# Kernel tuning notes

Measured on AMD Instinct MI355X. Metric: run time of the kernel, lower is better.

Reference implementation:

```python
import jax, jax.numpy as jnp
import numpy as np

L, B, T, TC, T1, D, DK, FF = 4, 4, 1024, 1024, 2048, 384, 256, 1536
TT = 0.1   # lamed blending coefficient (tt in (0,1] path)
EPS = 1e-5


def _ln(x, g, b):
    m = jnp.mean(x, axis=-1, keepdims=True)
    v = jnp.mean((x - m) ** 2, axis=-1, keepdims=True)
    return (x - m) * jax.lax.rsqrt(v + EPS) * g + b


def setup_inputs() -> dict:
    key = jax.random.key(0)
    ks = jax.random.split(key, 16)
    s = 0.02
    return {
        "tgt": jax.random.normal(ks[0], (B, T, D), jnp.float32),
        "memory": jax.random.normal(ks[1], (B, T1, DK), jnp.float32),
        "score_c": jax.random.normal(ks[2], (L, B, TC, T1), jnp.float32),
        "out_c": jax.random.normal(ks[3], (L, B, TC, D), jnp.float32),
        "Wq": jax.random.normal(ks[4], (L, D, D), jnp.float32) * s,
        "bq": jnp.zeros((L, D), jnp.float32),
        "Wk": jax.random.normal(ks[5], (L, D, DK), jnp.float32) * s,
        "bk": jnp.zeros((L, D), jnp.float32),
        "Wv": jax.random.normal(ks[6], (L, D, DK), jnp.float32) * s,
        "bv": jnp.zeros((L, D), jnp.float32),
        "Wkn": jax.random.normal(ks[7], (L, D, D), jnp.float32) * s,
        "bkn": jnp.zeros((L, D), jnp.float32),
        "Wun": jax.random.normal(ks[8], (L, D, D), jnp.float32) * s,
        "bun": jnp.zeros((L, D), jnp.float32),
        "W1": jax.random.normal(ks[9], (L, FF, D), jnp.float32) * s,
        "b1": jnp.zeros((L, FF), jnp.float32),
        "W2": jax.random.normal(ks[10], (L, D, FF), jnp.float32) * s,
        "b2": jnp.zeros((L, D), jnp.float32),
        "g1": jnp.ones((L, D), jnp.float32),
        "be1": jnp.zeros((L, D), jnp.float32),
        "g2": jnp.ones((L, D), jnp.float32),
        "be2": jnp.zeros((L, D), jnp.float32),
    }


def reference(tgt, memory, score_c, out_c, Wq, bq, Wk, bk, Wv, bv,
              Wkn, bkn, Wun, bun, W1, b1, W2, b2, g1, be1, g2, be2):
    scale = 1.0 / np.sqrt(D)
    x = tgt
    for l in range(L):  # fixed small layer count
        # cross-attention q/k/v (n_head = 1)
        q = jnp.einsum('btd,ed->bte', x, Wq[l]) + bq[l]            # [B,T,D]
        k = jnp.einsum('bsk,ek->bse', memory, Wk[l]) + bk[l]       # [B,T1,D]
        v = jnp.einsum('bsk,ek->bse', memory, Wv[l]) + bv[l]       # [B,T1,D]
        att = jnp.einsum('bte,bse->bts', q, k) * scale             # [B,T,T1]
        # blended score path (tt in (0,1])
        unk = jnp.einsum('btd,ed->bte', x, Wun[l]) + bun[l]        # [B,T,D]
        kno = jnp.einsum('bcd,ed->bce', out_c[l], Wkn[l]) + bkn[l] # [B,TC,D]
        score1 = jnp.einsum('bte,bce->btc', unk, kno) * scale      # [B,T,TC]
        mixed = jnp.einsum('btc,bcs->bts', score1, score_c[l])     # [B,T,T1]
        blended = TT * jax.nn.softmax(mixed, axis=-1) \
                  + (1.0 - TT) * jax.nn.softmax(att, axis=-1)
        z = jnp.einsum('bts,bse->bte', blended, v)                 # [B,T,D]
        x = _ln(x + z, g1[l], be1[l])
        h = jax.nn.relu(jnp.einsum('btd,fd->btf', x, W1[l]) + b1[l])
        y2 = jnp.einsum('btf,df->btd', h, W2[l]) + b2[l]
        x = _ln(x + y2, g2[l], be2[l])
    return x
```

## Files before the change

kernel.cpp:

```cpp
#include <hip/hip_runtime.h>
#include <math.h>

#define Lc 4
#define Bc 4
#define Tc 1024
#define TCc 1024
#define T1c 2048
#define Dc 384
#define DKc 256
#define FFc 1536
#define TTc 0.1f
#define EPSc 1e-5f

typedef unsigned short u16;
typedef __attribute__((ext_vector_type(8))) __bf16 bf16x8;
typedef __attribute__((ext_vector_type(8))) _Float16 f16x8;
typedef __attribute__((ext_vector_type(4))) float f32x4;

__device__ inline u16 f2bf(float f) {
  union { float f; unsigned u; } x; x.f = f;
  unsigned r = x.u + 0x7fffu + ((x.u >> 16) & 1u);
  return (u16)(r >> 16);
}

struct CDesc { const float* src; u16* dst; long n4; };
struct CPack { CDesc d[16]; long tot4; int nd; };

__global__ void cvt_multi(CPack P) {
  long i = (long)blockIdx.x * 256 + threadIdx.x;
  const long st = (long)gridDim.x * 256;
  for (; i < P.tot4; i += st) {
    long r = i; int g = 0;
    while (g < P.nd - 1 && r >= P.d[g].n4) { r -= P.d[g].n4; ++g; }
    float4 v = ((const float4*)P.d[g].src)[r];
    ushort4 o;
    o.x = f2bf(v.x); o.y = f2bf(v.y); o.z = f2bf(v.z); o.w = f2bf(v.w);
    ((ushort4*)P.d[g].dst)[r] = o;
  }
}

__global__ void concat_bias(const float* __restrict__ a, const float* __restrict__ b,
                            float* __restrict__ o) {
  int l = blockIdx.x, t = threadIdx.x;
  o[l * 768 + t] = (t < Dc) ? a[l * Dc + t] : b[l * Dc + t - Dc];
}

__global__ __launch_bounds__(256) void transpose_cvt(const float* __restrict__ src,
                                                     u16* __restrict__ dst) {
  __shared__ float t[64 * 65];
  const int z = blockIdx.z;
  const float* s = src + (long)z * TCc * T1c;
  u16* d = dst + (long)z * T1c * TCc;
  const int s0 = blockIdx.x * 64, c0 = blockIdx.y * 64;
  const int tc = threadIdx.x >> 4;
  const int tx = (threadIdx.x & 15) * 4;
#pragma unroll
  for (int it = 0; it < 4; ++it) {
    const int c = tc + it * 16;
    float4 v = *(const float4*)(s + (long)(c0 + c) * T1c + s0 + tx);
    float* q = t + c * 65 + tx;
    q[0] = v.x; q[1] = v.y; q[2] = v.z; q[3] = v.w;
  }
  __syncthreads();
#pragma unroll
  for (int it = 0; it < 4; ++it) {
    const int srow = tc + it * 16;
    u16 o[4];
#pragma unroll
    for (int k2 = 0; k2 < 4; ++k2) o[k2] = f2bf(t[(tx + k2) * 65 + srow]);
    *(ushort4*)(d + (long)(s0 + srow) * TCc + c0 + tx) = *(ushort4*)o;
  }
}

template<int BIAS_MODE, int RELU, int OUT_MODE, int SWIZ, int DUAL>
__global__ __launch_bounds__(256) void gemm_bt(
    const u16* __restrict__ A, const u16* __restrict__ B,
    void* __restrict__ C, const float* __restrict__ bias,
    float alpha, int N, int K, int lda, int ldb,
    long sA, long sB, long sC, long sBias, int ksplit, long sSlab, int bdivA,
    const u16* __restrict__ B2, int ldb2, long sB2, int aoff2,
    void* __restrict__ C2, float alpha2, int nbat)
{
  __shared__ __attribute__((aligned(16))) u16 As[2][128 * 32];
  __shared__ __attribute__((aligned(16))) u16 Bs[2][128 * 32];
  const int bz = blockIdx.z;
  int b = bz / ksplit;
  const int kc = bz - b * ksplit;
  const u16* Bp = B; int ldbv = ldb; long sBv = sB; void* Cp = C;
  int aoff = 0; float al = alpha;
  if (DUAL && b >= nbat) {
    b -= nbat; Bp = B2; ldbv = ldb2; sBv = sB2; Cp = C2; aoff = aoff2; al = alpha2;
  }
  const int ba = b / bdivA;
  const int Klen = K / ksplit;
  const int k0 = kc * Klen;
  const u16* Ab = A + (long)ba * sA + aoff;
  const u16* Bb = Bp + (long)b * sBv;
  long tm, tn;
  if (SWIZ) {
    const int id = blockIdx.y * 16 + blockIdx.x;
    tm = (long)(id >> 4) * 128;
    tn = (long)(2 * (id & 7) + ((id >> 3) & 1)) * 128;
  } else {
    tm = (long)blockIdx.y * 128; tn = (long)blockIdx.x * 128;
  }
  const int tid = threadIdx.x;
  const int lane = tid & 63, wv = tid >> 6;
  const int wm = (wv >> 1) * 64, wn = (wv & 1) * 64;
  const int q = lane >> 4, r = lane & 15;
  const int ldr = lane >> 2;
  const int ldc = (lane & 3) * 8;

  const u16* gA0 = Ab + (tm + wv * 32 + ldr) * (long)lda + k0 + ldc;
  const u16* gA1 = gA0 + 16 * (long)lda;
  const u16* gB0 = Bb + (tn + wv * 32 + ldr) * (long)ldbv + k0 + ldc;
  const u16* gB1 = gB0 + 16 * (long)ldbv;
  const int dof = (wv * 32 + ldr) * 32 + ldc;

  const f32x4 zero4 = {0.0f, 0.0f, 0.0f, 0.0f};
  f32x4 acc[4][4];
#pragma unroll
  for (int i = 0; i < 4; ++i)
#pragma unroll
    for (int j = 0; j < 4; ++j) acc[i][j] = zero4;

  uint4 ra0 = *(const uint4*)gA0;
  uint4 ra1 = *(const uint4*)gA1;
  uint4 rb0 = *(const uint4*)gB0;
  uint4 rb1 = *(const uint4*)gB1;

  const int iters = Klen >> 5;
  int cur = 0;
  for (int it = 0; it < iters; ++it) {
    u16* a0 = As[cur] + dof;
    u16* b0 = Bs[cur] + dof;
    *(uint4*)a0 = ra0; *(uint4*)(a0 + 512) = ra1;
    *(uint4*)b0 = rb0; *(uint4*)(b0 + 512) = rb1;
    if (it + 1 < iters) {
      const long o = (long)(it + 1) * 32;
      ra0 = *(const uint4*)(gA0 + o);
      ra1 = *(const uint4*)(gA1 + o);
      rb0 = *(const uint4*)(gB0 + o);
      rb1 = *(const uint4*)(gB1 + o);
    }
    __syncthreads();
    bf16x8 af[4], bfr[4];
#pragma unroll
    for (int i = 0; i < 4; ++i) {
      af[i]  = *(const bf16x8*)(As[cur] + (wm + i * 16 + r) * 32 + q * 8);
      bfr[i] = *(const bf16x8*)(Bs[cur] + (wn + i * 16 + r) * 32 + q * 8);
    }
#pragma unroll
    for (int i = 0; i < 4; ++i)
#pragma unroll
      for (int j = 0; j < 4; ++j)
        acc[i][j] = __builtin_amdgcn_mfma_f32_16x16x32_bf16(af[i], bfr[j], acc[i][j], 0, 0, 0);
    cur ^= 1;
  }

  const float* biasb = bias ? bias + (long)ba * sBias : nullptr;
#pragma unroll
  for (int i = 0; i < 4; ++i)
#pragma unroll
    for (int j = 0; j < 4; ++j)
#pragma unroll
      for (int v = 0; v < 4; ++v) {
        long row = tm + wm + i * 16 + q * 4 + v;
        long col = tn + wn + j * 16 + r;
        float val = acc[i][j][v] * al;
        if (BIAS_MODE == 1 && kc == 0) val += biasb[col];
        if (BIAS_MODE == 2 && kc == 0) val += biasb[row];
        if (RELU) val = fmaxf(val, 0.0f);
        long idx = (long)kc * sSlab + (long)b * sC + row * (long)N + col;
        if (OUT_MODE == 0)      ((float*)Cp)[idx] = val;
        else if (OUT_MODE == 1) ((u16*)Cp)[idx] = f2bf(val);
        else                    ((_Float16*)Cp)[idx] = (_Float16)val;
      }
}

__global__ __launch_bounds__(256) void blend_softmax(
    const _Float16* __restrict__ att, const _Float16* __restrict__ mixed,
    u16* __restrict__ out)
{
  const long row = blockIdx.x;
  const int tid = threadIdx.x;
  f16x8 av = *(const f16x8*)(att + row * T1c + tid * 8);
  f16x8 mv = *(const f16x8*)(mixed + row * T1c + tid * 8);
  float a[8], m[8];
#pragma unroll
  for (int i = 0; i < 8; ++i) { a[i] = (float)av[i]; m[i] = (float)mv[i]; }
  float amax = a[0], mmax = m[0];
#pragma unroll
  for (int i = 1; i < 8; ++i) { amax = fmaxf(amax, a[i]); mmax = fmaxf(mmax, m[i]); }
#pragma unroll
  for (int off = 32; off > 0; off >>= 1) {
    amax = fmaxf(amax, __shfl_xor(amax, off));
    mmax = fmaxf(mmax, __shfl_xor(mmax, off));
  }
  __shared__ float red[8];
  const int lane = tid & 63, wv = tid >> 6;
  if (lane == 0) { red[wv] = amax; red[4 + wv] = mmax; }
  __syncthreads();
  amax = fmaxf(fmaxf(red[0], red[1]), fmaxf(red[2], red[3]));
  mmax = fmaxf(fmaxf(red[4], red[5]), fmaxf(red[6], red[7]));
  __syncthreads();
  float asum = 0.f, msum = 0.f;
#pragma unroll
  for (int i = 0; i < 8; ++i) {
    a[i] = __expf(a[i] - amax); asum += a[i];
    m[i] = __expf(m[i] - mmax); msum += m[i];
  }
#pragma unroll
  for (int off = 32; off > 0; off >>= 1) {
    asum += __shfl_xor(asum, off);
    msum += __shfl_xor(msum, off);
  }
  if (lane == 0) { red[wv] = asum; red[4 + wv] = msum; }
  __syncthreads();
  asum = red[0] + red[1] + red[2] + red[3];
  msum = red[4] + red[5] + red[6] + red[7];
  const float ca = (1.0f - TTc) / asum, cm = TTc / msum;
  u16 o[8];
#pragma unroll
  for (int i = 0; i < 8; ++i) o[i] = f2bf(a[i] * ca + m[i] * cm);
  *(uint4*)(out + row * T1c + tid * 8) = *(uint4*)o;
}

__global__ __launch_bounds__(384) void add_ln4(
    const float* __restrict__ xin, const float* __restrict__ zs,
    const float* __restrict__ g, const float* __restrict__ be,
    float* __restrict__ xout, u16* __restrict__ xbf)
{
  const long row = blockIdx.x;
  const int d = threadIdx.x;
  const long SL = (long)Bc * Tc * Dc;
  const long o = row * Dc + d;
  float v = xin[o] + zs[o] + zs[SL + o] + zs[2 * SL + o] + zs[3 * SL + o];
  float s = v, s2 = v * v;
#pragma unroll
  for (int off = 32; off > 0; off >>= 1) {
    s  += __shfl_xor(s, off);
    s2 += __shfl_xor(s2, off);
  }
  __shared__ float red[12];
  const int lane = d & 63, wv = d >> 6;
  if (lane == 0) { red[wv] = s; red[6 + wv] = s2; }
  __syncthreads();
  float S = 0.f, S2 = 0.f;
#pragma unroll
  for (int w = 0; w < 6; ++w) { S += red[w]; S2 += red[6 + w]; }
  const float mean = S * (1.0f / Dc);
  const float var  = S2 * (1.0f / Dc) - mean * mean;
  const float rstd = rsqrtf(var + EPSc);
  const float y = (v - mean) * rstd * g[d] + be[d];
  xout[o] = y;
  xbf[o] = f2bf(y);
}

extern "C" void kernel_launch(void* const* d_in, const int* in_sizes, int n_in,
                              void* d_out, int out_size, void* d_ws, size_t ws_size,
                              hipStream_t stream)
{
  const float* tgt     = (const float*)d_in[0];
  const float* memory  = (const float*)d_in[1];
  const float* score_c = (const float*)d_in[2];
  const float* out_c   = (const float*)d_in[3];
  const float* Wq  = (const float*)d_in[4];  const float* bq  = (const float*)d_in[5];
  const float* Wk  = (const float*)d_in[6];  const float* bk  = (const float*)d_in[7];
  const float* Wv  = (const float*)d_in[8];  const float* bv  = (const float*)d_in[9];
  const float* Wkn = (const float*)d_in[10]; const float* bkn = (const float*)d_in[11];
  const float* Wun = (const float*)d_in[12]; const float* bun = (const float*)d_in[13];
  const float* W1  = (const float*)d_in[14]; const float* b1  = (const float*)d_in[15];
  const float* W2  = (const float*)d_in[16]; const float* b2  = (const float*)d_in[17];
  const float* g1  = (const float*)d_in[18]; const float* be1 = (const float*)d_in[19];
  const float* g2  = (const float*)d_in[20]; const float* be2 = (const float*)d_in[21];
  (void)in_sizes; (void)n_in; (void)out_size;

  char* p = (char*)d_ws;
  auto alloc = [&](size_t b) { char* r = p; p += (b + 255) & ~(size_t)255; return r; };

  u16* wk_bf   = (u16*)alloc((size_t)Lc * Dc * DKc * 2);
  u16* wv_bf   = (u16*)alloc((size_t)Lc * Dc * DKc * 2);
  u16* wkn_bf  = (u16*)alloc((size_t)Lc * Dc * Dc * 2);
  u16* w1_bf   = (u16*)alloc((size_t)Lc * FFc * Dc * 2);
  u16* w2_bf   = (u16*)alloc((size_t)Lc * Dc * FFc * 2);
  u16* wqu_bf  = (u16*)alloc((size_t)Lc * 2 * Dc * Dc * 2);
  float* bqu   = (float*)alloc((size_t)Lc * 2 * Dc * 4);
  u16* mem_bf  = (u16*)alloc((size_t)Bc * T1c * DKc * 2);
  u16* outc_bf = (u16*)alloc((size_t)Lc * Bc * TCc * Dc * 2);
  u16* x_bf    = (u16*)alloc((size_t)Bc * Tc * Dc * 2);
  float* xbuf  = (float*)alloc((size_t)Bc * Tc * Dc * 4);
  u16* qunk_bf = (u16*)alloc((size_t)Bc * Tc * 2 * Dc * 2);
  u16* k_all   = (u16*)alloc((size_t)Bc * T1c * Lc * Dc * 2);
  u16* vT_all  = (u16*)alloc((size_t)Bc * Lc * Dc * T1c * 2);
  u16* knoT_all = (u16*)alloc((size_t)Lc * Bc * Dc * TCc * 2);
  u16* M2T_all = (u16*)alloc((size_t)Lc * Bc * T1c * Dc * 2);
  u16* scT_all = (u16*)alloc((size_t)Lc * Bc * T1c * TCc * 2);
  _Float16* att   = (_Float16*)alloc((size_t)Bc * Tc * T1c * 2);
  _Float16* mixed = (_Float16*)alloc((size_t)Bc * Tc * T1c * 2);
  u16* blended = (u16*)alloc((size_t)Bc * Tc * T1c * 2);
  float* zslab = (float*)alloc((size_t)4 * Bc * Tc * Dc * 4);
  float* yslab = (float*)alloc((size_t)4 * Bc * Tc * Dc * 4);
  u16* h_bf    = (u16*)alloc((size_t)Bc * Tc * FFc * 2);

  if ((size_t)(p - (char*)d_ws) > ws_size) return;

  {
    CPack cp{}; int g = 0; long tot4 = 0;
    auto add = [&](const float* s, u16* d, long n) {
      cp.d[g].src = s; cp.d[g].dst = d; cp.d[g].n4 = n / 4; tot4 += n / 4; ++g;
    };
    add(Wk,  wk_bf,  (long)Lc * Dc * DKc);
    add(Wv,  wv_bf,  (long)Lc * Dc * DKc);
    add(Wkn, wkn_bf, (long)Lc * Dc * Dc);
    add(W1,  w1_bf,  (long)Lc * FFc * Dc);
    add(W2,  w2_bf,  (long)Lc * Dc * FFc);
    add(memory, mem_bf, (long)Bc * T1c * DKc);
    add(out_c, outc_bf, (long)Lc * Bc * TCc * Dc);
    add(tgt, x_bf, (long)Bc * Tc * Dc);
    for (int l = 0; l < Lc; ++l) {
      add(Wq + (long)l * Dc * Dc,  wqu_bf + (long)l * 2 * Dc * Dc, (long)Dc * Dc);
      add(Wun + (long)l * Dc * Dc, wqu_bf + (long)l * 2 * Dc * Dc + Dc * Dc, (long)Dc * Dc);
    }
    cp.nd = g; cp.tot4 = tot4;
    cvt_multi<<<4096, 256, 0, stream>>>(cp);
  }
  concat_bias<<<Lc, 2 * Dc, 0, stream>>>(bq, bun, bqu);

  transpose_cvt<<<dim3(T1c / 64, TCc / 64, Lc * Bc), 256, 0, stream>>>(score_c, scT_all);

  const float scale = 1.0f / sqrtf((float)Dc);
  const long SLAB = (long)Bc * Tc * Dc;

  gemm_bt<1,0,1,0,0><<<dim3(Lc*Dc/128, Bc*T1c/128, 1), 256, 0, stream>>>(
      mem_bf, wk_bf, k_all, bk, 1.0f, Lc*Dc, DKc, DKc, DKc, 0, 0, 0, 0, 1, 0, 1,
      nullptr, 0, 0, 0, nullptr, 0.f, 0);
  gemm_bt<2,0,1,0,0><<<dim3(T1c/128, Lc*Dc/128, Bc), 256, 0, stream>>>(
      wv_bf, mem_bf, vT_all, bv, 1.0f, T1c, DKc, DKc, DKc,
      0, (long)T1c*DKc, (long)Lc*Dc*T1c, 0, 1, 0, 1,
      nullptr, 0, 0, 0, nullptr, 0.f, 0);
  gemm_bt<2,0,1,0,0><<<dim3(TCc/128, Dc/128, Lc*Bc), 256, 0, stream>>>(
      wkn_bf, outc_bf, knoT_all, bkn, 1.0f, TCc, Dc, Dc, Dc,
      (long)Dc*Dc, (long)TCc*Dc, (long)Dc*TCc, Dc, 1, 0, Bc,
      nullptr, 0, 0, 0, nullptr, 0.f, 0);
  gemm_bt<0,0,1,0,0><<<dim3(Dc/128, T1c/128, Lc*Bc), 256, 0, stream>>>(
      scT_all, knoT_all, M2T_all, nullptr, scale, Dc, TCc, TCc, TCc,
      (long)T1c*TCc, (long)Dc*TCc, (long)T1c*Dc, 0, 1, 0, 1,
      nullptr, 0, 0, 0, nullptr, 0.f, 0);

  for (int l = 0; l < Lc; ++l) {
    gemm_bt<1,0,1,0,0><<<dim3(2*Dc/128, Bc*Tc/128, 1), 256, 0, stream>>>(
        x_bf, wqu_bf + (long)l*2*Dc*Dc, qunk_bf, bqu + l*2*Dc,
        1.0f, 2*Dc, Dc, Dc, Dc, 0, 0, 0, 0, 1, 0, 1,
        nullptr, 0, 0, 0, nullptr, 0.f, 0);
    gemm_bt<0,0,2,1,1><<<dim3(T1c/128, Tc/128, 2*Bc), 256, 0, stream>>>(
        qunk_bf, k_all + l*Dc, att, nullptr, scale, T1c, Dc, 2*Dc, Lc*Dc,
        (long)Tc*2*Dc, (long)T1c*Lc*Dc, (long)Tc*T1c, 0, 1, 0, 1,
        M2T_all + (long)l*Bc*T1c*Dc, Dc, (long)T1c*Dc, Dc, mixed, 1.0f, Bc);
    blend_softmax<<<Bc*Tc, 256, 0, stream>>>(att, mixed, blended);
    gemm_bt<0,0,0,0,0><<<dim3(Dc/128, Tc/128, Bc*4), 256, 0, stream>>>(
        blended, vT_all + (long)l*Dc*T1c, zslab, nullptr, 1.0f,
        Dc, T1c, T1c, T1c, (long)Tc*T1c, (long)Lc*Dc*T1c, (long)Tc*Dc, 0, 4, SLAB, 1,
        nullptr, 0, 0, 0, nullptr, 0.f, 0);
    add_ln4<<<Bc*Tc, Dc, 0, stream>>>(
        (l == 0) ? tgt : xbuf, zslab, g1 + l*Dc, be1 + l*Dc, xbuf, x_bf);
    gemm_bt<1,1,1,0,0><<<dim3(FFc/128, Bc*Tc/128, 1), 256, 0, stream>>>(
        x_bf, w1_bf + (long)l*FFc*Dc, h_bf, b1 + l*FFc, 1.0f,
        FFc, Dc, Dc, Dc, 0, 0, 0, 0, 1, 0, 1,
        nullptr, 0, 0, 0, nullptr, 0.f, 0);
    gemm_bt<1,0,0,0,0><<<dim3(Dc/128, Bc*Tc/128, 4), 256, 0, stream>>>(
        h_bf, w2_bf + (long)l*Dc*FFc, yslab, b2 + l*Dc, 1.0f,
        Dc, FFc, FFc, FFc, 0, 0, 0, 0, 4, SLAB, 1,
        nullptr, 0, 0, 0, nullptr, 0.f, 0);
    add_ln4<<<Bc*Tc, Dc, 0, stream>>>(
        xbuf, yslab, g2 + l*Dc, be2 + l*Dc,
        (l == Lc - 1) ? (float*)d_out : xbuf, x_bf);
  }
}
```

Before: 953.0 us.

## Fold Wk into Wq so attention scores contract directly against memory

The query and key projections are merged algebraically. A per-layer combined weight Wq^T·Wk (384x256) and a bias bq·Wk are precomputed, so the score GEMM multiplies the projected queries directly against bf16 memory. This removes the large K projection GEMM and its k_all buffer, and shrinks the contraction length of the att half of the dual score GEMM from 384 to 256. The fused QU projection also narrows from 768 to 640 columns. The bk-dependent terms are dropped because they are constant along the softmax axis. The catch is extra transposes and a small precompute GEMM, one more bf16 rounding of the fused weight, and uneven K between the two halves of the dual GEMM.

```diff
diff --git a/kernel.cpp b/kernel.cpp
--- a/kernel.cpp
+++ b/kernel.cpp
@@ -11,6 +11,7 @@
 #define FFc 1536
 #define TTc 0.1f
 #define EPSc 1e-5f
+#define QUc 640
 
 typedef unsigned short u16;
 typedef __attribute__((ext_vector_type(8))) __bf16 bf16x8;
@@ -21,6 +22,9 @@
   union { float f; unsigned u; } x; x.f = f;
   unsigned r = x.u + 0x7fffu + ((x.u >> 16) & 1u);
   return (u16)(r >> 16);
+}
+__device__ inline float bf2f(u16 v) {
+  union { unsigned u; float f; } x; x.u = (unsigned)v << 16; return x.f;
 }
 
 struct CDesc { const float* src; u16* dst; long n4; };
@@ -39,25 +43,34 @@
   }
 }
 
-__global__ void concat_bias(const float* __restrict__ a, const float* __restrict__ b,
-                            float* __restrict__ o) {
-  int l = blockIdx.x, t = threadIdx.x;
-  o[l * 768 + t] = (t < Dc) ? a[l * Dc + t] : b[l * Dc + t - Dc];
+__global__ void make_bias(const float* __restrict__ bq, const float* __restrict__ bun,
+                          const u16* __restrict__ wkT, float* __restrict__ bqu) {
+  const int l = blockIdx.x, t = threadIdx.x;
+  if (t < DKc) {
+    const u16* w = wkT + ((long)l * DKc + t) * Dc;
+    const float* b = bq + l * Dc;
+    float s = 0.f;
+    for (int e = 0; e < Dc; ++e) s += b[e] * bf2f(w[e]);
+    bqu[l * QUc + t] = s;
+  } else {
+    bqu[l * QUc + t] = bun[l * Dc + (t - DKc)];
+  }
 }
 
 __global__ __launch_bounds__(256) void transpose_cvt(const float* __restrict__ src,
-                                                     u16* __restrict__ dst) {
+                                                     u16* __restrict__ dst,
+                                                     int R, int C) {
   __shared__ float t[64 * 65];
   const int z = blockIdx.z;
-  const float* s = src + (long)z * TCc * T1c;
-  u16* d = dst + (long)z * T1c * TCc;
+  const float* s = src + (long)z * R * C;
+  u16* d = dst + (long)z * R * C;
   const int s0 = blockIdx.x * 64, c0 = blockIdx.y * 64;
   const int tc = threadIdx.x >> 4;
   const int tx = (threadIdx.x & 15) * 4;
 #pragma unroll
   for (int it = 0; it < 4; ++it) {
     const int c = tc + it * 16;
-    float4 v = *(const float4*)(s + (long)(c0 + c) * T1c + s0 + tx);
+    float4 v = *(const float4*)(s + (long)(c0 + c) * C + s0 + tx);
     float* q = t + c * 65 + tx;
     q[0] = v.x; q[1] = v.y; q[2] = v.z; q[3] = v.w;
   }
@@ -68,7 +81,7 @@
     u16 o[4];
 #pragma unroll
     for (int k2 = 0; k2 < 4; ++k2) o[k2] = f2bf(t[(tx + k2) * 65 + srow]);
-    *(ushort4*)(d + (long)(s0 + srow) * TCc + c0 + tx) = *(ushort4*)o;
+    *(ushort4*)(d + (long)(s0 + srow) * R + c0 + tx) = *(ushort4*)o;
   }
 }
 
@@ -79,7 +92,7 @@
     float alpha, int N, int K, int lda, int ldb,
     long sA, long sB, long sC, long sBias, int ksplit, long sSlab, int bdivA,
     const u16* __restrict__ B2, int ldb2, long sB2, int aoff2,
-    void* __restrict__ C2, float alpha2, int nbat)
+    void* __restrict__ C2, float alpha2, int nbat, int K2)
 {
   __shared__ __attribute__((aligned(16))) u16 As[2][128 * 32];
   __shared__ __attribute__((aligned(16))) u16 Bs[2][128 * 32];
@@ -87,12 +100,13 @@
   int b = bz / ksplit;
   const int kc = bz - b * ksplit;
   const u16* Bp = B; int ldbv = ldb; long sBv = sB; void* Cp = C;
-  int aoff = 0; float al = alpha;
+  int aoff = 0; float al = alpha; int Kv = K;
   if (DUAL && b >= nbat) {
-    b -= nbat; Bp = B2; ldbv = ldb2; sBv = sB2; Cp = C2; aoff = aoff2; al = alpha2;
+    b -= nbat; Bp = B2; ldbv = ldb2; sBv = sB2; Cp = C2;
+    aoff = aoff2; al = alpha2; Kv = K2;
   }
   const int ba = b / bdivA;
-  const int Klen = K / ksplit;
+  const int Klen = Kv / ksplit;
   const int k0 = kc * Klen;
   const u16* Ab = A + (long)ba * sA + aoff;
   const u16* Bb = Bp + (long)b * sBv;
@@ -274,24 +288,24 @@
   const float* W2  = (const float*)d_in[16]; const float* b2  = (const float*)d_in[17];
   const float* g1  = (const float*)d_in[18]; const float* be1 = (const float*)d_in[19];
   const float* g2  = (const float*)d_in[20]; const float* be2 = (const float*)d_in[21];
-  (void)in_sizes; (void)n_in; (void)out_size;
+  (void)bk; (void)in_sizes; (void)n_in; (void)out_size;
 
   char* p = (char*)d_ws;
   auto alloc = [&](size_t b) { char* r = p; p += (b + 255) & ~(size_t)255; return r; };
 
-  u16* wk_bf   = (u16*)alloc((size_t)Lc * Dc * DKc * 2);
   u16* wv_bf   = (u16*)alloc((size_t)Lc * Dc * DKc * 2);
   u16* wkn_bf  = (u16*)alloc((size_t)Lc * Dc * Dc * 2);
   u16* w1_bf   = (u16*)alloc((size_t)Lc * FFc * Dc * 2);
   u16* w2_bf   = (u16*)alloc((size_t)Lc * Dc * FFc * 2);
-  u16* wqu_bf  = (u16*)alloc((size_t)Lc * 2 * Dc * Dc * 2);
-  float* bqu   = (float*)alloc((size_t)Lc * 2 * Dc * 4);
+  u16* wqT     = (u16*)alloc((size_t)Lc * Dc * Dc * 2);
+  u16* wkT     = (u16*)alloc((size_t)Lc * DKc * Dc * 2);
+  u16* wqu_bf  = (u16*)alloc((size_t)Lc * QUc * Dc * 2);
+  float* bqu   = (float*)alloc((size_t)Lc * QUc * 4);
   u16* mem_bf  = (u16*)alloc((size_t)Bc * T1c * DKc * 2);
   u16* outc_bf = (u16*)alloc((size_t)Lc * Bc * TCc * Dc * 2);
   u16* x_bf    = (u16*)alloc((size_t)Bc * Tc * Dc * 2);
   float* xbuf  = (float*)alloc((size_t)Bc * Tc * Dc * 4);
-  u16* qunk_bf = (u16*)alloc((size_t)Bc * Tc * 2 * Dc * 2);
-  u16* k_all   = (u16*)alloc((size_t)Bc * T1c * Lc * Dc * 2);
+  u16* qunk_bf = (u16*)alloc((size_t)Bc * Tc * QUc * 2);
   u16* vT_all  = (u16*)alloc((size_t)Bc * Lc * Dc * T1c * 2);
   u16* knoT_all = (u16*)alloc((size_t)Lc * Bc * Dc * TCc * 2);
   u16* M2T_all = (u16*)alloc((size_t)Lc * Bc * T1c * Dc * 2);
@@ -310,7 +324,6 @@
     auto add = [&](const float* s, u16* d, long n) {
       cp.d[g].src = s; cp.d[g].dst = d; cp.d[g].n4 = n / 4; tot4 += n / 4; ++g;
     };
-    add(Wk,  wk_bf,  (long)Lc * Dc * DKc);
     add(Wv,  wv_bf,  (long)Lc * Dc * DKc);
     add(Wkn, wkn_bf, (long)Lc * Dc * Dc);
     add(W1,  w1_bf,  (long)Lc * FFc * Dc);
@@ -318,60 +331,64 @@
     add(memory, mem_bf, (long)Bc * T1c * DKc);
     add(out_c, outc_bf, (long)Lc * Bc * TCc * Dc);
     add(tgt, x_bf, (long)Bc * Tc * Dc);
-    for (int l = 0; l < Lc; ++l) {
-      add(Wq + (long)l * Dc * Dc,  wqu_bf + (long)l * 2 * Dc * Dc, (long)Dc * Dc);
-      add(Wun + (long)l * Dc * Dc, wqu_bf + (long)l * 2 * Dc * Dc + Dc * Dc, (long)Dc * Dc);
-    }
+    for (int l = 0; l < Lc; ++l)
+      add(Wun + (long)l * Dc * Dc,
+          wqu_bf + (long)l * QUc * Dc + (long)DKc * Dc, (long)Dc * Dc);
     cp.nd = g; cp.tot4 = tot4;
     cvt_multi<<<4096, 256, 0, stream>>>(cp);
   }
-  concat_bias<<<Lc, 2 * Dc, 0, stream>>>(bq, bun, bqu);
-
-  transpose_cvt<<<dim3(T1c / 64, TCc / 64, Lc * Bc), 256, 0, stream>>>(score_c, scT_all);
+
+  transpose_cvt<<<dim3(T1c / 64, TCc / 64, Lc * Bc), 256, 0, stream>>>(
+      score_c, scT_all, TCc, T1c);
+  transpose_cvt<<<dim3(Dc / 64, Dc / 64, Lc), 256, 0, stream>>>(Wq, wqT, Dc, Dc);
+  transpose_cvt<<<dim3(DKc / 64, Dc / 64, Lc), 256, 0, stream>>>(Wk, wkT, Dc, DKc);
 
   const float scale = 1.0f / sqrtf((float)Dc);
   const long SLAB = (long)Bc * Tc * Dc;
 
-  gemm_bt<1,0,1,0,0><<<dim3(Lc*Dc/128, Bc*T1c/128, 1), 256, 0, stream>>>(
-      mem_bf, wk_bf, k_all, bk, 1.0f, Lc*Dc, DKc, DKc, DKc, 0, 0, 0, 0, 1, 0, 1,
-      nullptr, 0, 0, 0, nullptr, 0.f, 0);
+  gemm_bt<0,0,1,0,0><<<dim3(Dc/128, DKc/128, Lc), 256, 0, stream>>>(
+      wkT, wqT, wqu_bf, nullptr, 1.0f, Dc, Dc, Dc, Dc,
+      (long)DKc*Dc, (long)Dc*Dc, (long)QUc*Dc, 0, 1, 0, 1,
+      nullptr, 0, 0, 0, nullptr, 0.f, 0, Dc);
+  make_bias<<<Lc, QUc, 0, stream>>>(bq, bun, wkT, bqu);
+
   gemm_bt<2,0,1,0,0><<<dim3(T1c/128, Lc*Dc/128, Bc), 256, 0, stream>>>(
       wv_bf, mem_bf, vT_all, bv, 1.0f, T1c, DKc, DKc, DKc,
       0, (long)T1c*DKc, (long)Lc*Dc*T1c, 0, 1, 0, 1,
-      nullptr, 0, 0, 0, nullptr, 0.f, 0);
+      nullptr, 0, 0, 0, nullptr, 0.f, 0, DKc);
   gemm_bt<2,0,1,0,0><<<dim3(TCc/128, Dc/128, Lc*Bc), 256, 0, stream>>>(
       wkn_bf, outc_bf, knoT_all, bkn, 1.0f, TCc, Dc, Dc, Dc,
       (long)Dc*Dc, (long)TCc*Dc, (long)Dc*TCc, Dc, 1, 0, Bc,
-      nullptr, 0, 0, 0, nullptr, 0.f, 0);
+      nullptr, 0, 0, 0, nullptr, 0.f, 0, Dc);
   gemm_bt<0,0,1,0,0><<<dim3(Dc/128, T1c/128, Lc*Bc), 256, 0, stream>>>(
       scT_all, knoT_all, M2T_all, nullptr, scale, Dc, TCc, TCc, TCc,
       (long)T1c*TCc, (long)Dc*TCc, (long)T1c*Dc, 0, 1, 0, 1,
-      nullptr, 0, 0, 0, nullptr, 0.f, 0);
+      nullptr, 0, 0, 0, nullptr, 0.f, 0, TCc);
 
   for (int l = 0; l < Lc; ++l) {
-    gemm_bt<1,0,1,0,0><<<dim3(2*Dc/128, Bc*Tc/128, 1), 256, 0, stream>>>(
-        x_bf, wqu_bf + (long)l*2*Dc*Dc, qunk_bf, bqu + l*2*Dc,
-        1.0f, 2*Dc, Dc, Dc, Dc, 0, 0, 0, 0, 1, 0, 1,
-        nullptr, 0, 0, 0, nullptr, 0.f, 0);
+    gemm_bt<1,0,1,0,0><<<dim3(QUc/128, Bc*Tc/128, 1), 256, 0, stream>>>(
+        x_bf, wqu_bf + (long)l*QUc*Dc, qunk_bf, bqu + l*QUc,
+        1.0f, QUc, Dc, Dc, Dc, 0, 0, 0, 0, 1, 0, 1,
+        nullptr, 0, 0, 0, nullptr, 0.f, 0, Dc);
     gemm_bt<0,0,2,1,1><<<dim3(T1c/128, Tc/128, 2*Bc), 256, 0, stream>>>(
-        qunk_bf, k_all + l*Dc, att, nullptr, scale, T1c, Dc, 2*Dc, Lc*Dc,
-        (long)Tc*2*Dc, (long)T1c*Lc*Dc, (long)Tc*T1c, 0, 1, 0, 1,
-        M2T_all + (long)l*Bc*T1c*Dc, Dc, (long)T1c*Dc, Dc, mixed, 1.0f, Bc);
+        qunk_bf, mem_bf, att, nullptr, scale, T1c, DKc, QUc, DKc,
+        (long)Tc*QUc, (long)T1c*DKc, (long)Tc*T1c, 0, 1, 0, 1,
+        M2T_all + (long)l*Bc*T1c*Dc, Dc, (long)T1c*Dc, DKc, mixed, 1.0f, Bc, Dc);
     blend_softmax<<<Bc*Tc, 256, 0, stream>>>(att, mixed, blended);
     gemm_bt<0,0,0,0,0><<<dim3(Dc/128, Tc/128, Bc*4), 256, 0, stream>>>(
         blended, vT_all + (long)l*Dc*T1c, zslab, nullptr, 1.0f,
         Dc, T1c, T1c, T1c, (long)Tc*T1c, (long)Lc*Dc*T1c, (long)Tc*Dc, 0, 4, SLAB, 1,
-        nullptr, 0, 0, 0, nullptr, 0.f, 0);
+        nullptr, 0, 0, 0, nullptr, 0.f, 0, T1c);
     add_ln4<<<Bc*Tc, Dc, 0, stream>>>(
         (l == 0) ? tgt : xbuf, zslab, g1 + l*Dc, be1 + l*Dc, xbuf, x_bf);
     gemm_bt<1,1,1,0,0><<<dim3(FFc/128, Bc*Tc/128, 1), 256, 0, stream>>>(
         x_bf, w1_bf + (long)l*FFc*Dc, h_bf, b1 + l*FFc, 1.0f,
         FFc, Dc, Dc, Dc, 0, 0, 0, 0, 1, 0, 1,
-        nullptr, 0, 0, 0, nullptr, 0.f, 0);
+        nullptr, 0, 0, 0, nullptr, 0.f, 0, Dc);
     gemm_bt<1,0,0,0,0><<<dim3(Dc/128, Bc*Tc/128, 4), 256, 0, stream>>>(
         h_bf, w2_bf + (long)l*Dc*FFc, yslab, b2 + l*Dc, 1.0f,
         Dc, FFc, FFc, FFc, 0, 0, 0, 0, 4, SLAB, 1,
-        nullptr, 0, 0, 0, nullptr, 0.f, 0);
+        nullptr, 0, 0, 0, nullptr, 0.f, 0, FFc);
     add_ln4<<<Bc*Tc, Dc, 0, stream>>>(
         xbuf, yslab, g2 + l*Dc, be2 + l*Dc,
         (l == Lc - 1) ? (float*)d_out : xbuf, x_bf);
```

Result: no change. 939.2 us (-1.4%).
